# Optimization experiments

Hardware: AMD Instinct MI355X
Metric: run time of the kernel (lower is better)

The kernel has to match this reference:

```python
import jax, jax.numpy as jnp
import numpy as np

NEG_INF = -1.0e9
LN_EPS = 1e-5
LEAK = 0.2


def setup_inputs() -> dict:
    key = jax.random.key(0)
    ks = jax.random.split(key, 8)
    B, C, T, N, H = 8, 64, 24, 512, 2
    hd = C // H
    x = jax.random.normal(ks[0], (B, C, T, N), dtype=jnp.float32)
    gso = jax.random.randint(ks[1], (N, N), 0, 2, dtype=jnp.int32)
    # torch nn.Linear weights are (out, in); xavier-ish scale
    s = (2.0 / (C + C)) ** 0.5
    Wq = jax.random.normal(ks[2], (C, C), dtype=jnp.float32) * s
    Wk = jax.random.normal(ks[3], (C, C), dtype=jnp.float32) * s
    Wv = jax.random.normal(ks[4], (C, C), dtype=jnp.float32) * s
    sa = (2.0 / (H + hd)) ** 0.5
    a_src = jax.random.normal(ks[5], (H, hd), dtype=jnp.float32) * sa
    a_dst = jax.random.normal(ks[6], (H, hd), dtype=jnp.float32) * sa
    ln_gamma = jnp.ones((C,), dtype=jnp.float32)
    ln_beta = jnp.zeros((C,), dtype=jnp.float32)
    return {"x": x, "gso": gso, "Wq": Wq, "Wk": Wk, "Wv": Wv,
            "a_src": a_src, "a_dst": a_dst, "ln_gamma": ln_gamma, "ln_beta": ln_beta}


def _spatial_gat(x, gso, Wq, Wk, Wv, a_src, a_dst, ln_gamma, ln_beta):
    B, C, T, N = x.shape
    H, hd = a_src.shape
    # (B, C, T, N) -> (B*T, N, C)
    xr = jnp.transpose(x, (0, 2, 3, 1)).reshape(B * T, N, C)
    # torch Linear: y = x @ W.T
    Q = jnp.einsum('bnc,dc->bnd', xr, Wq).reshape(B * T, N, H, hd)
    K = jnp.einsum('bnc,dc->bnd', xr, Wk).reshape(B * T, N, H, hd)
    V = jnp.einsum('bnc,dc->bnd', xr, Wv).reshape(B * T, N, H, hd)
    # additive GAT scores, all heads at once
    s_src = jnp.einsum('bnhd,hd->bnh', Q, a_src)  # (BT, N, H)
    s_dst = jnp.einsum('bnhd,hd->bnh', K, a_dst)  # (BT, N, H)
    scores = jax.nn.leaky_relu(s_src[:, :, None, :] + s_dst[:, None, :, :], LEAK)  # (BT, Ni, Nj, H)
    mask = jnp.where(gso == 0, jnp.float32(NEG_INF), jnp.float32(0.0))  # (N, N)
    scores = scores + mask[None, :, :, None]
    attn = jax.nn.softmax(scores, axis=2)  # softmax over destination j
    out = jnp.einsum('bijh,bjhd->bihd', attn, V)  # (BT, N, H, hd)
    out = out.reshape(B * T, N, C)
    # LayerNorm over channel dim
    mu = jnp.mean(out, axis=-1, keepdims=True)
    var = jnp.var(out, axis=-1, keepdims=True)
    out = (out - mu) * jax.lax.rsqrt(var + LN_EPS) * ln_gamma + ln_beta
    # back to (B, C, T, N)
    return jnp.transpose(out.reshape(B, T, N, C), (0, 3, 1, 2))


def reference(x, gso, Wq, Wk, Wv, a_src, a_dst, ln_gamma, ln_beta):
    return _spatial_gat(x, gso, Wq, Wk, Wv, a_src, a_dst, ln_gamma, ln_beta)
```

## Files before the change

### kernel.cpp

```cpp
#include <hip/hip_runtime.h>

#define CDIM 64
#define TDIM 24
#define NDIM 512
#define NBT  192

typedef float    float4v __attribute__((ext_vector_type(4)));
typedef _Float16 half8v  __attribute__((ext_vector_type(8)));
typedef _Float16 half4v  __attribute__((ext_vector_type(4)));
typedef _Float16 half2v  __attribute__((ext_vector_type(2)));


__device__ __forceinline__ float exp2_fast(float x) {
#if __has_builtin(__builtin_amdgcn_exp2f)
  return __builtin_amdgcn_exp2f(x);
#else
  return __expf(x * 0.69314718f);
#endif
}

__device__ __forceinline__ half8v ld8(const _Float16* p) {
  half4v a = *(const half4v*)p;
  half4v b = *(const half4v*)(p + 4);
  return __builtin_shufflevector(a, b, 0, 1, 2, 3, 4, 5, 6, 7);
}

__global__ void k0_prep(const int* __restrict__ gso,
                        const float* __restrict__ Wq, const float* __restrict__ Wk,
                        const float* __restrict__ Wv,
                        const float* __restrict__ a_src, const float* __restrict__ a_dst,
                        unsigned* __restrict__ maskb, _Float16* __restrict__ wvext_g) {
  int t = threadIdx.x;
  if (blockIdx.x < 256) {
    int tg = blockIdx.x * 256 + t;
    int4 g = ((const int4*)gso)[tg];
    unsigned w = (g.x ? 0x000000FFu : 0u) | (g.y ? 0x0000FF00u : 0u) |
                 (g.z ? 0x00FF0000u : 0u) | (g.w ? 0xFF000000u : 0u);
    maskb[tg] = w;
  } else {
    for (int idx = t; idx < 80 * 68; idx += 256) {
      int row = idx / 68, col = idx - row * 68;
      float v = 0.f;
      if (col < 64) {
        if (row < 64) {
          v = Wv[row * 64 + col];
        } else if (row < 68) {
          int r = row - 64;
          const float* av = (r & 2) ? a_dst : a_src;
          const float* W  = (r & 2) ? Wk : Wq;
          int off = (r & 1) * 32;
          float s = 0.f;
#pragma unroll
          for (int d = 0; d < 32; ++d)
            s += av[off + d] * W[(off + d) * 64 + col];
          v = s * 1.44269504f;
        }
      }
      wvext_g[idx] = (_Float16)v;
    }
  }
}

struct SmemK1 {
  union {
    _Float16 xt[128][68];
    _Float16 vtb[64][136];
  } big;
  _Float16 wvext[80][68];
};

__launch_bounds__(256, 4)
__global__ void k1_v(const float* __restrict__ x, const _Float16* __restrict__ wvext_g,
                     _Float16* __restrict__ VT_g,
                     float* __restrict__ s_src_g, float* __restrict__ s_dst_g) {
  __shared__ SmemK1 sm;
  const int t  = threadIdx.x;
  const int qn = blockIdx.x;
  const int bt = blockIdx.y;
  const int b  = bt / TDIM, tt = bt % TDIM;
  const int n0 = qn * 128;

  {
    const uint4* wsrc = (const uint4*)wvext_g;
    uint4* wdst = (uint4*)sm.wvext;
#pragma unroll
    for (int it = 0; it < 3; ++it) {
      int idx = it * 256 + t;
      if (idx < 680) wdst[idx] = wsrc[idx];
    }
  }
  for (int it = 0; it < 16; ++it) {
    int idx = it * 256 + t;
    int cp = idx >> 7, n = idx & 127;
    int c0 = cp * 2;
    const float* base = x + ((size_t)(b * CDIM + c0) * TDIM + tt) * NDIM + n0 + n;
    half2v p; p[0] = (_Float16)base[0]; p[1] = (_Float16)base[(size_t)TDIM * NDIM];
    *(half2v*)&sm.big.xt[n][c0] = p;
  }
  __syncthreads();

  const int lane = t & 63, w = t >> 6;
  const int m = lane & 15, quad = lane >> 4;
  const int mbase = w * 32;

  float4v acc[2][5];
#pragma unroll
  for (int mt = 0; mt < 2; ++mt)
#pragma unroll
    for (int nt = 0; nt < 5; ++nt)
#pragma unroll
      for (int r = 0; r < 4; ++r) acc[mt][nt][r] = 0.f;

#pragma unroll
  for (int ks = 0; ks < 2; ++ks) {
    half8v af[2], bf[5];
#pragma unroll
    for (int mt = 0; mt < 2; ++mt)
      af[mt] = ld8(&sm.big.xt[mbase + mt * 16 + m][ks * 32 + quad * 8]);
#pragma unroll
    for (int nt = 0; nt < 4; ++nt)
      bf[nt] = ld8(&sm.wvext[nt * 16 + m][ks * 32 + quad * 8]);
    bf[4] = ld8(&sm.wvext[64 + m][ks * 32 + quad * 8]);
#pragma unroll
    for (int mt = 0; mt < 2; ++mt)
#pragma unroll
      for (int nt = 0; nt < 5; ++nt)
        acc[mt][nt] = __builtin_amdgcn_mfma_f32_16x16x32_f16(af[mt], bf[nt], acc[mt][nt], 0, 0, 0);
  }

  if (m < 4) {
    float* basep = (m < 2 ? s_src_g : s_dst_g) + (size_t)(bt * 2 + (m & 1)) * NDIM;
#pragma unroll
    for (int mt = 0; mt < 2; ++mt)
#pragma unroll
      for (int r = 0; r < 4; ++r)
        basep[n0 + mbase + mt * 16 + quad * 4 + r] = acc[mt][4][r];
  }
  __syncthreads();

#pragma unroll
  for (int mt = 0; mt < 2; ++mt)
#pragma unroll
    for (int nt = 0; nt < 4; ++nt)
#pragma unroll
      for (int r = 0; r < 4; r += 2) {
        int nl = mbase + mt * 16 + quad * 4 + r;
        int c  = nt * 16 + m;
        half2v p = __builtin_bit_cast(half2v,
            __builtin_amdgcn_cvt_pkrtz(acc[mt][nt][r], acc[mt][nt][r + 1]));
        *(half2v*)&sm.big.vtb[c][nl] = p;
      }
  __syncthreads();

  const unsigned* vdw = (const unsigned*)sm.big.vtb;
  unsigned* outdw = (unsigned*)VT_g;
  for (int it = 0; it < 16; ++it) {
    int idx = it * 256 + t;
    int c = idx >> 6, jd = idx & 63;
    outdw[(size_t)(bt * 64 + c) * 256 + qn * 64 + jd] = vdw[c * 68 + jd];
  }
}

struct SmemK2 {
  union {
    struct { _Float16 vt[64][128]; unsigned char mb[64][144]; } s;
    struct { float otile[64][66]; float rsum[4][64]; float rsq[4][64];
             float mu[64]; float rs[64]; } e;
  } u;
  _Float16 sF16[2][512];
  _Float16 sP16[2][512];
};

__launch_bounds__(256, 4)
__global__ void k2_attn(const _Float16* __restrict__ VT_g,
                        const float* __restrict__ s_src_g, const float* __restrict__ s_dst_g,
                        const unsigned char* __restrict__ maskb,
                        const float* __restrict__ gamma, const float* __restrict__ beta,
                        float* __restrict__ out) {
  __shared__ SmemK2 sm;
  const int t     = threadIdx.x;
  const int itile = blockIdx.x;
  const int bt    = blockIdx.y;
  const int i0    = itile * 64;
  const int b     = bt / TDIM, tt = bt % TDIM;
  const int lane  = t & 63, w = t >> 6;
  const int h = w >> 1, ihalf = w & 1;
  const int m = lane & 15, quad = lane >> 4;

  for (int it = 0; it < 4; ++it) {
    int idx = it * 256 + t;
    float d = s_dst_g[(size_t)bt * 2 * NDIM + idx];
    ((_Float16*)sm.sF16)[idx] = (_Float16)exp2_fast(d);
    ((_Float16*)sm.sP16)[idx] = (_Float16)exp2_fast(0.2f * d);
  }
  half8v E8[2], Q8[2];
#pragma unroll
  for (int mt = 0; mt < 2; ++mt) {
    float sv = s_src_g[(size_t)(bt * 2 + h) * NDIM + i0 + ihalf * 32 + mt * 16 + m];
    _Float16 ev = (_Float16)exp2_fast(sv - 6.f);
    _Float16 qv = (_Float16)exp2_fast(0.2f * sv - 6.f);
#pragma unroll
    for (int jj = 0; jj < 8; ++jj) { E8[mt][jj] = ev; Q8[mt][jj] = qv; }
  }

  float4v acc[2][2], accs[2];
#pragma unroll
  for (int mt = 0; mt < 2; ++mt) {
#pragma unroll
    for (int r = 0; r < 4; ++r) { acc[mt][0][r] = 0.f; acc[mt][1][r] = 0.f; accs[mt][r] = 0.f; }
  }
  const half8v bones = {(_Float16)1.f, (_Float16)1.f, (_Float16)1.f, (_Float16)1.f,
                        (_Float16)1.f, (_Float16)1.f, (_Float16)1.f, (_Float16)1.f};

  for (int js = 0; js < 4; ++js) {
    __syncthreads();
    {
      const uint4* vsrc = (const uint4*)VT_g;
#pragma unroll
      for (int it = 0; it < 4; ++it) {
        int idx = it * 256 + t;
        int c = idx >> 4, ch = idx & 15;
        uint4 val = vsrc[(size_t)(bt * 64 + c) * 64 + js * 16 + ch];
        *(uint4*)&sm.u.s.vt[c][(ch * 8) ^ ((c & 7) * 8)] = val;
      }
#pragma unroll
      for (int it = 0; it < 2; ++it) {
        int idx = it * 256 + t;
        int c = idx >> 3, ch = idx & 7;
        uint4 mv = *(const uint4*)(maskb + (size_t)(i0 + c) * NDIM + js * 128 + ch * 16);
        *(uint4*)&sm.u.s.mb[c][ch * 16] = mv;
      }
    }
    __syncthreads();

#pragma unroll
    for (int ksl = 0; ksl < 4; ++ksl) {
      int jq = ksl * 32 + quad * 8;
      half8v F8 = *(const half8v*)&sm.sF16[h][js * 128 + jq];
      half8v P8 = *(const half8v*)&sm.sP16[h][js * 128 + jq];
      int vbase = (h * 32 + m) * 128 + (jq ^ ((m & 7) * 8));
      half8v b0 = *(const half8v*)&sm.u.s.vt[0][vbase];
      half8v b1 = *(const half8v*)&sm.u.s.vt[0][vbase + 16 * 128];
#pragma unroll
      for (int mt = 0; mt < 2; ++mt) {
        const unsigned* mwp = (const unsigned*)&sm.u.s.mb[ihalf * 32 + mt * 16 + m][jq];
        unsigned mw0 = mwp[0], mw1 = mwp[1];
        half8v e8 = __builtin_elementwise_max(E8[mt] * F8, Q8[mt] * P8);
        uint4 eu = __builtin_bit_cast(uint4, e8);
        eu.x &= __builtin_amdgcn_perm(0u, mw0, 0x01010000u);
        eu.y &= __builtin_amdgcn_perm(0u, mw0, 0x03030202u);
        eu.z &= __builtin_amdgcn_perm(0u, mw1, 0x01010000u);
        eu.w &= __builtin_amdgcn_perm(0u, mw1, 0x03030202u);
        half8v af = __builtin_bit_cast(half8v, eu);
        acc[mt][0] = __builtin_amdgcn_mfma_f32_16x16x32_f16(af, b0,    acc[mt][0], 0, 0, 0);
        acc[mt][1] = __builtin_amdgcn_mfma_f32_16x16x32_f16(af, b1,    acc[mt][1], 0, 0, 0);
        accs[mt]   = __builtin_amdgcn_mfma_f32_16x16x32_f16(af, bones, accs[mt],   0, 0, 0);
      }
    }
  }

  __syncthreads();
#pragma unroll
  for (int mt = 0; mt < 2; ++mt)
#pragma unroll
    for (int r = 0; r < 4; ++r) {
      float sc = __builtin_amdgcn_rcpf(accs[mt][r]);
      int i_loc = ihalf * 32 + mt * 16 + quad * 4 + r;
#pragma unroll
      for (int nt = 0; nt < 2; ++nt)
        sm.u.e.otile[i_loc][h * 32 + nt * 16 + m] = acc[mt][nt][r] * sc;
    }
  __syncthreads();

  {
    int i = t & 63, cg = t >> 6;
    float s1 = 0.f, s2 = 0.f;
#pragma unroll
    for (int cc = 0; cc < 16; ++cc) {
      float v = sm.u.e.otile[i][cg * 16 + cc];
      s1 += v; s2 += v * v;
    }
    sm.u.e.rsum[cg][i] = s1;
    sm.u.e.rsq[cg][i]  = s2;
  }
  __syncthreads();
  if (t < 64) {
    int i = t;
    float s1 = 0.f, s2 = 0.f;
#pragma unroll
    for (int cg = 0; cg < 4; ++cg) { s1 += sm.u.e.rsum[cg][i]; s2 += sm.u.e.rsq[cg][i]; }
    float mu  = s1 * (1.f / 64.f);
    float var = s2 * (1.f / 64.f) - mu * mu;
    sm.u.e.mu[i] = mu;
    sm.u.e.rs[i] = rsqrtf(var + 1e-5f);
  }
  __syncthreads();
  {
    int i = t & 63, cg = t >> 6;
    float mu = sm.u.e.mu[i], rs = sm.u.e.rs[i];
    int n = i0 + i;
#pragma unroll
    for (int cc = 0; cc < 16; ++cc) {
      int c = cg * 16 + cc;
      float v = (sm.u.e.otile[i][c] - mu) * rs * gamma[c] + beta[c];
      out[((size_t)(b * CDIM + c) * TDIM + tt) * NDIM + n] = v;
    }
  }
}

extern "C" void kernel_launch(void* const* d_in, const int* in_sizes, int n_in,
                              void* d_out, int out_size, void* d_ws, size_t ws_size,
                              hipStream_t stream) {
  const float* x     = (const float*)d_in[0];
  const int*   gso   = (const int*)d_in[1];
  const float* Wq    = (const float*)d_in[2];
  const float* Wk    = (const float*)d_in[3];
  const float* Wv    = (const float*)d_in[4];
  const float* a_src = (const float*)d_in[5];
  const float* a_dst = (const float*)d_in[6];
  const float* gamma = (const float*)d_in[7];
  const float* beta  = (const float*)d_in[8];
  float* out = (float*)d_out;

  char* ws = (char*)d_ws;
  _Float16* VT_g  = (_Float16*)ws;
  float*    s_src = (float*)(ws + 12582912);
  float*    s_dst = (float*)(ws + 13369344);
  unsigned char* maskb = (unsigned char*)(ws + 14155776);
  _Float16* wvext = (_Float16*)(ws + 14417920);

  k0_prep<<<257, 256, 0, stream>>>(gso, Wq, Wk, Wv, a_src, a_dst, (unsigned*)maskb, wvext);
  k1_v<<<dim3(4, NBT), 256, 0, stream>>>(x, wvext, VT_g, s_src, s_dst);
  k2_attn<<<dim3(8, NBT), 256, 0, stream>>>(VT_g, s_src, s_dst, maskb, gamma, beta, out);
}
```

Before: 135.3 us.

## Fold prep kernel into V-projection kernel and widen LDS row padding

```diff
diff --git a/kernel.cpp b/kernel.cpp
--- a/kernel.cpp
+++ b/kernel.cpp
@@ -19,75 +19,65 @@
 #endif
 }
 
-__device__ __forceinline__ half8v ld8(const _Float16* p) {
-  half4v a = *(const half4v*)p;
-  half4v b = *(const half4v*)(p + 4);
-  return __builtin_shufflevector(a, b, 0, 1, 2, 3, 4, 5, 6, 7);
-}
-
-__global__ void k0_prep(const int* __restrict__ gso,
-                        const float* __restrict__ Wq, const float* __restrict__ Wk,
-                        const float* __restrict__ Wv,
-                        const float* __restrict__ a_src, const float* __restrict__ a_dst,
-                        unsigned* __restrict__ maskb, _Float16* __restrict__ wvext_g) {
-  int t = threadIdx.x;
-  if (blockIdx.x < 256) {
-    int tg = blockIdx.x * 256 + t;
-    int4 g = ((const int4*)gso)[tg];
-    unsigned w = (g.x ? 0x000000FFu : 0u) | (g.y ? 0x0000FF00u : 0u) |
-                 (g.z ? 0x00FF0000u : 0u) | (g.w ? 0xFF000000u : 0u);
-    maskb[tg] = w;
-  } else {
-    for (int idx = t; idx < 80 * 68; idx += 256) {
-      int row = idx / 68, col = idx - row * 68;
-      float v = 0.f;
-      if (col < 64) {
-        if (row < 64) {
-          v = Wv[row * 64 + col];
-        } else if (row < 68) {
-          int r = row - 64;
-          const float* av = (r & 2) ? a_dst : a_src;
-          const float* W  = (r & 2) ? Wk : Wq;
-          int off = (r & 1) * 32;
-          float s = 0.f;
-#pragma unroll
-          for (int d = 0; d < 32; ++d)
-            s += av[off + d] * W[(off + d) * 64 + col];
-          v = s * 1.44269504f;
-        }
-      }
-      wvext_g[idx] = (_Float16)v;
-    }
-  }
-}
-
 struct SmemK1 {
   union {
-    _Float16 xt[128][68];
+    _Float16 xt[128][72];
     _Float16 vtb[64][136];
   } big;
-  _Float16 wvext[80][68];
+  _Float16 wv[64][72];
+  _Float16 wext[16][72];
 };
 
 __launch_bounds__(256, 4)
-__global__ void k1_v(const float* __restrict__ x, const _Float16* __restrict__ wvext_g,
+__global__ void k1_v(const float* __restrict__ x,  const float* __restrict__ Wv,
+                     const float* __restrict__ Wq, const float* __restrict__ Wk,
+                     const float* __restrict__ a_src, const float* __restrict__ a_dst,
+                     const int* __restrict__ gso,
                      _Float16* __restrict__ VT_g,
-                     float* __restrict__ s_src_g, float* __restrict__ s_dst_g) {
+                     float* __restrict__ s_src_g, float* __restrict__ s_dst_g,
+                     unsigned char* __restrict__ maskb) {
+  const int t  = threadIdx.x;
+  const int bx = blockIdx.x;
+
+  if (bx >= 768) {
+    int g = (bx - 768) * 256 + t;
+    const int4* gp = (const int4*)gso + (size_t)g * 4;
+    unsigned w[4];
+#pragma unroll
+    for (int k = 0; k < 4; ++k) {
+      int4 v = gp[k];
+      w[k] = (v.x ? 0x000000FFu : 0u) | (v.y ? 0x0000FF00u : 0u) |
+             (v.z ? 0x00FF0000u : 0u) | (v.w ? 0xFF000000u : 0u);
+    }
+    uint4 o; o.x = w[0]; o.y = w[1]; o.z = w[2]; o.w = w[3];
+    ((uint4*)maskb)[g] = o;
+    return;
+  }
+
   __shared__ SmemK1 sm;
-  const int t  = threadIdx.x;
-  const int qn = blockIdx.x;
-  const int bt = blockIdx.y;
+  const int qn = bx & 3;
+  const int bt = bx >> 2;
   const int b  = bt / TDIM, tt = bt % TDIM;
   const int n0 = qn * 128;
 
-  {
-    const uint4* wsrc = (const uint4*)wvext_g;
-    uint4* wdst = (uint4*)sm.wvext;
-#pragma unroll
-    for (int it = 0; it < 3; ++it) {
-      int idx = it * 256 + t;
-      if (idx < 680) wdst[idx] = wsrc[idx];
-    }
+  for (int it = 0; it < 16; ++it) {
+    int idx = it * 256 + t;
+    sm.wv[idx >> 6][idx & 63] = (_Float16)Wv[idx];
+  }
+  for (int z = t; z < 12 * 72; z += 256) ((_Float16*)sm.wext[4])[z] = (_Float16)0.f;
+  if (t < 64) {
+    int c = t;
+    float s0 = 0.f, s1 = 0.f, d0 = 0.f, d1 = 0.f;
+#pragma unroll
+    for (int d = 0; d < 32; ++d) {
+      s0 += a_src[d]      * Wq[d * 64 + c];
+      s1 += a_src[32 + d] * Wq[(32 + d) * 64 + c];
+      d0 += a_dst[d]      * Wk[d * 64 + c];
+      d1 += a_dst[32 + d] * Wk[(32 + d) * 64 + c];
+    }
+    const float l2e = 1.44269504f;
+    sm.wext[0][c] = (_Float16)(s0 * l2e); sm.wext[1][c] = (_Float16)(s1 * l2e);
+    sm.wext[2][c] = (_Float16)(d0 * l2e); sm.wext[3][c] = (_Float16)(d1 * l2e);
   }
   for (int it = 0; it < 16; ++it) {
     int idx = it * 256 + t;
@@ -116,11 +106,11 @@
     half8v af[2], bf[5];
 #pragma unroll
     for (int mt = 0; mt < 2; ++mt)
-      af[mt] = ld8(&sm.big.xt[mbase + mt * 16 + m][ks * 32 + quad * 8]);
+      af[mt] = *(const half8v*)&sm.big.xt[mbase + mt * 16 + m][ks * 32 + quad * 8];
 #pragma unroll
     for (int nt = 0; nt < 4; ++nt)
-      bf[nt] = ld8(&sm.wvext[nt * 16 + m][ks * 32 + quad * 8]);
-    bf[4] = ld8(&sm.wvext[64 + m][ks * 32 + quad * 8]);
+      bf[nt] = *(const half8v*)&sm.wv[nt * 16 + m][ks * 32 + quad * 8];
+    bf[4] = *(const half8v*)&sm.wext[m][ks * 32 + quad * 8];
 #pragma unroll
     for (int mt = 0; mt < 2; ++mt)
 #pragma unroll
@@ -327,9 +317,8 @@
   float*    s_src = (float*)(ws + 12582912);
   float*    s_dst = (float*)(ws + 13369344);
   unsigned char* maskb = (unsigned char*)(ws + 14155776);
-  _Float16* wvext = (_Float16*)(ws + 14417920);
-
-  k0_prep<<<257, 256, 0, stream>>>(gso, Wq, Wk, Wv, a_src, a_dst, (unsigned*)maskb, wvext);
-  k1_v<<<dim3(4, NBT), 256, 0, stream>>>(x, wvext, VT_g, s_src, s_dst);
+
+  k1_v<<<832, 256, 0, stream>>>(x, Wv, Wq, Wk, a_src, a_dst, gso,
+                                VT_g, s_src, s_dst, maskb);
   k2_attn<<<dim3(8, NBT), 256, 0, stream>>>(VT_g, s_src, s_dst, maskb, gamma, beta, out);
 }
```

Measured after the change: 128.8 us. -4.8%, faster.
